# Performance work log

Measured on AMD Instinct MI355X. Metric: run time of the kernel, lower is better.

The kernel has to match this reference:

```python
import jax, jax.numpy as jnp
import numpy as np

B, T, C = 2, 2048, 1024
H = 16
D = C // H
E = 16
K = 2
THETA = 10000.0
ALPHA = 0.01
EPS = 1e-5


def rmsnorm(x, w):
    ms = jnp.mean(jnp.square(x), axis=-1, keepdims=True)
    return x * jax.lax.rsqrt(ms + EPS) * w


def rope_cos_sin(t_len, dim):
    # matches precompute_freqs_cis: freqs = theta**(-2i/dim), angles = t * freqs
    freqs = 1.0 / THETA ** (jnp.arange(0, dim // 2, dtype=jnp.float32) * 2.0 / dim)
    ang = jnp.arange(t_len, dtype=jnp.float32)[:, None] * freqs[None, :]  # [T, D/2]
    return jnp.cos(ang), jnp.sin(ang)


def apply_rope(x, cos, sin):
    # x: [B,T,H,D]; complex rotation on consecutive pairs (view_as_complex semantics)
    xr = x.reshape(x.shape[:-1] + (D // 2, 2))
    x0, x1 = xr[..., 0], xr[..., 1]
    c = cos[None, :, None, :]
    s = sin[None, :, None, :]
    return jnp.stack([x0 * c - x1 * s, x0 * s + x1 * c], axis=-1).reshape(x.shape)


def mlp(x, wf, bf, wp, bp):
    return jax.nn.silu(x @ wf + bf) @ wp + bp


def setup_inputs() -> dict:
    key = jax.random.key(0)
    ks = jax.random.split(key, 16)
    s = 0.02
    return {
        'x': jax.random.normal(ks[0], (B, T, C), jnp.float32),
        'ln1_w': jax.random.normal(ks[1], (C,), jnp.float32),
        'ln2_w': jax.random.normal(ks[2], (C,), jnp.float32),
        'w_attn': jax.random.normal(ks[3], (C, 3 * C), jnp.float32) * s,
        'b_attn': jnp.zeros((3 * C,), jnp.float32),
        'w_proj': jax.random.normal(ks[4], (C, C), jnp.float32) * s,
        'b_proj': jnp.zeros((C,), jnp.float32),
        'gate_w': jax.random.normal(ks[5], (E, C), jnp.float32) * s,
        'gate_bias': jnp.zeros((E,), jnp.float32),
        'exp_wf': jax.random.normal(ks[6], (E, C, 2 * C), jnp.float32) * s,
        'exp_bf': jnp.zeros((E, 2 * C), jnp.float32),
        'exp_wp': jax.random.normal(ks[7], (E, 2 * C, C), jnp.float32) * s,
        'exp_bp': jnp.zeros((E, C), jnp.float32),
        'sh_wf': jax.random.normal(ks[8], (C, 2 * C), jnp.float32) * s,
        'sh_bf': jnp.zeros((2 * C,), jnp.float32),
        'sh_wp': jax.random.normal(ks[9], (2 * C, C), jnp.float32) * s,
        'sh_bp': jnp.zeros((C,), jnp.float32),
    }


def reference(x, ln1_w, ln2_w, w_attn, b_attn, w_proj, b_proj, gate_w, gate_bias,
              exp_wf, exp_bf, exp_wp, exp_bp, sh_wf, sh_bf, sh_wp, sh_bp):
    # ---- attention sub-block ----
    h = rmsnorm(x, ln1_w)
    qkv = h @ w_attn + b_attn  # [B,T,3C]
    q, k, v = jnp.split(qkv, 3, axis=-1)
    q = q.reshape(B, T, H, D)
    k = k.reshape(B, T, H, D)
    v = v.reshape(B, T, H, D)
    cos, sin = rope_cos_sin(T, D)
    q = apply_rope(q, cos, sin)
    k = apply_rope(k, cos, sin)
    scores = jnp.einsum('bqhd,bkhd->bhqk', q, k) / jnp.sqrt(jnp.float32(D))
    causal = jnp.tril(jnp.ones((T, T), dtype=bool))
    scores = jnp.where(causal, scores, -jnp.inf)
    attn = jax.nn.softmax(scores, axis=-1)
    y = jnp.einsum('bhqk,bkhd->bqhd', attn, v).reshape(B, T, C)
    x = x + y @ w_proj + b_proj
    # ---- MoE sub-block ----
    h = rmsnorm(x, ln2_w).reshape(-1, C)  # [N,C]
    N = h.shape[0]
    logits = h @ gate_w.T
    p = jax.nn.softmax(logits.astype(jnp.float32), axis=-1)  # original_scores [N,E]
    _, idx = jax.lax.top_k(p + gate_bias, K)  # topk on biased scores
    w_sel = jnp.take_along_axis(p, idx, axis=-1)  # weights from unbiased scores [N,K]
    onehot = jax.nn.one_hot(idx, E, dtype=p.dtype)  # [N,K,E]
    w_dense = jnp.sum(onehot * w_sel[..., None], axis=1)  # [N,E] combine weights
    counts = jnp.sum(onehot, axis=(0, 1))  # bincount
    f_i = counts * E / (K * N + 1e-6)
    expert_probs = p.mean(axis=0)
    lb_loss = ALPHA * jnp.sum(f_i * expert_probs)
    out = jnp.zeros_like(h)
    for i in range(E):  # fixed small expert count
        out = out + mlp(h, exp_wf[i], exp_bf[i], exp_wp[i], exp_bp[i]) * w_dense[:, i:i + 1]
    out = out + mlp(h, sh_wf, sh_bf, sh_wp, sh_bp)
    return x + out.reshape(B, T, C), lb_loss
```

## Files before the change

kernel.cpp:

```cpp
#include <hip/hip_runtime.h>

typedef __bf16 bf16x8 __attribute__((ext_vector_type(8)));
typedef short  short8 __attribute__((ext_vector_type(8)));
typedef float  f32x4  __attribute__((ext_vector_type(4)));
typedef unsigned short u16;

#define NTOK 4096
#define TSEQ 2048
#define CDIM 1024
#define NEXP 16

__device__ __forceinline__ u16 f2bf(float f){
  union { float f; unsigned u; } v; v.f = f;
  unsigned r = v.u + 0x7fffu + ((v.u >> 16) & 1u);
  return (u16)(r >> 16);
}
__device__ __forceinline__ float bf2f(u16 u){
  union { unsigned u; float f; } v; v.u = ((unsigned)u) << 16; return v.f;
}

__device__ __forceinline__ f32x4 mfma16(short8 a, short8 b, f32x4 c){
  return __builtin_amdgcn_mfma_f32_16x16x32_bf16(
      __builtin_bit_cast(bf16x8, a), __builtin_bit_cast(bf16x8, b), c, 0, 0, 0);
}

__device__ __forceinline__ void gload_lds16(const void* g, void* l){
  __builtin_amdgcn_global_load_lds((__attribute__((address_space(1))) void*)g,
                                   (__attribute__((address_space(3))) void*)l,
                                   16, 0, 0);
}

__device__ __forceinline__ void tp_body(const float* __restrict__ in, u16* __restrict__ out,
                                        int K, int N, int k0, int n0, u16* lds16, int tid)
{
  int tx = tid & 15;
#pragma unroll
  for (int p = 0; p < 2; ++p) {
    int q = (tid >> 4) + p * 16;
    int k = 2 * q;
    float4 v0 = *(const float4*)(in + (size_t)(k0 + k)     * N + n0 + tx * 4);
    float4 v1 = *(const float4*)(in + (size_t)(k0 + k + 1) * N + n0 + tx * 4);
    const float* a0 = (const float*)&v0;
    const float* a1 = (const float*)&v1;
#pragma unroll
    for (int i = 0; i < 4; ++i) {
      unsigned val = (unsigned)f2bf(a0[i]) | ((unsigned)f2bf(a1[i]) << 16);
      *(unsigned*)&lds16[(tx * 4 + i) * 66 + k] = val;
    }
  }
  __syncthreads();
#pragma unroll
  for (int p = 0; p < 2; ++p) {
    int n = (tid >> 3) + p * 32;
    int k8 = (tid & 7) * 8;
    const unsigned* l32 = (const unsigned*)&lds16[n * 66 + k8];
    uint4 o4;
    o4.x = l32[0]; o4.y = l32[1]; o4.z = l32[2]; o4.w = l32[3];
    *(uint4*)(out + (size_t)(n0 + n) * K + k0 + k8) = o4;
  }
}

__global__ void transpose_wattn_k(const float* __restrict__ in, u16* __restrict__ out)
{
  __shared__ u16 lds16[64 * 66];
  int r = blockIdx.x;
  int n0 = (r % 48) * 64, k0 = (r / 48) * 64;
  tp_body(in, out, 1024, 3072, k0, n0, lds16, threadIdx.x);
}

__global__ void concat_bias_k(const float* __restrict__ exp_bf, const float* __restrict__ sh_bf,
                              const float* __restrict__ exp_bp, const float* __restrict__ sh_bp,
                              float* __restrict__ bf17, float* __restrict__ bp17)
{
  int i = blockIdx.x * 256 + threadIdx.x;
  if (i < 16 * 2048) bf17[i] = exp_bf[i];
  else if (i < 17 * 2048) bf17[i] = sh_bf[i - 16 * 2048];
  if (i < 16 * 1024) bp17[i] = exp_bp[i];
  else if (i < 17 * 1024) bp17[i] = sh_bp[i - 16 * 1024];
}

__global__ void rmsnorm_k(const float* __restrict__ x, const float* __restrict__ w,
                          u16* __restrict__ ob, float* __restrict__ of)
{
  int row = blockIdx.x, tid = threadIdx.x;
  const float4* xr = (const float4*)(x + (size_t)row * CDIM);
  float4 v = xr[tid];
  float ss = v.x*v.x + v.y*v.y + v.z*v.z + v.w*v.w;
  for (int d = 1; d < 64; d <<= 1) ss += __shfl_xor(ss, d);
  __shared__ float wacc[4];
  if ((tid & 63) == 0) wacc[tid >> 6] = ss;
  __syncthreads();
  float tot = wacc[0] + wacc[1] + wacc[2] + wacc[3];
  float scale = rsqrtf(tot * (1.0f / CDIM) + 1e-5f);
  float4 wv = ((const float4*)w)[tid];
  float o0 = v.x * scale * wv.x, o1 = v.y * scale * wv.y;
  float o2 = v.z * scale * wv.z, o3 = v.w * scale * wv.w;
  if (of) ((float4*)(of + (size_t)row * CDIM))[tid] = make_float4(o0, o1, o2, o3);
  ushort4 ov; ov.x = f2bf(o0); ov.y = f2bf(o1); ov.z = f2bf(o2); ov.w = f2bf(o3);
  ((ushort4*)(ob + (size_t)row * CDIM))[tid] = ov;
}

template<int MODE, int SWZ>
__global__ void __launch_bounds__(256, 4)
gemm_bt(const u16* __restrict__ A, int lda,
        const u16* __restrict__ Bt, long long bStrideZ,
        const float* __restrict__ bias, int biasStrideZ,
        void* __restrict__ Cout,
        const float* __restrict__ resid,
        int M, int N, int K,
        const int* __restrict__ counts, const int* __restrict__ offsets,
        const int* __restrict__ tokA, u16* __restrict__ vtp)
{
  int cb, rb, z;
  if (SWZ) {
    int nwg = gridDim.x * gridDim.y * gridDim.z;
    int d = (blockIdx.z * gridDim.y + blockIdx.y) * gridDim.x + blockIdx.x;
    int o = (d & 7) * (nwg >> 3) + (d >> 3);
    cb = o % gridDim.x;
    int t2 = o / gridDim.x;
    rb = t2 % gridDim.y;
    z  = t2 / gridDim.y;
  } else {
    cb = blockIdx.x; rb = blockIdx.y; z = blockIdx.z;
  }

  int mLoc = M, rowBase = 0;
  if (counts) { mLoc = counts[z]; rowBase = offsets[z]; }
  if (rb * 128 >= mLoc) return;

  const u16* Bz = Bt + (size_t)z * bStrideZ;
  const float* bz = bias + (size_t)z * biasStrideZ;

  __shared__ u16 lds_a[2][128 * 32];
  __shared__ u16 lds_b[2][128 * 32];

  int tid = threadIdx.x;
  int lane = tid & 63, wave = tid >> 6;
  int wm = wave >> 1, wn = wave & 1;
  int srow = wave * 16 + (lane >> 2);
  int skel = (lane & 3) * 8;
  int r16 = lane & 15, g8 = (lane >> 4) * 8;

  size_t arow[2];
  int ncol[2];
#pragma unroll
  for (int c = 0; c < 2; ++c) {
    int rloc = rb * 128 + c * 64 + srow;
    if (rloc >= mLoc) rloc = mLoc - 1;
    int grow = rowBase + rloc;
    arow[c] = tokA ? (size_t)tokA[grow] : (size_t)grow;
    ncol[c] = cb * 128 + c * 64 + srow;
  }

  f32x4 acc[4][4] = {};

  auto stage = [&](int kt, int buf){
    int k0 = kt * 32;
#pragma unroll
    for (int c = 0; c < 2; ++c) {
      gload_lds16(A + arow[c] * lda + k0 + skel,
                  (char*)&lds_a[buf][0] + c * 4096 + wave * 1024);
      gload_lds16(Bz + (size_t)ncol[c] * K + k0 + skel,
                  (char*)&lds_b[buf][0] + c * 4096 + wave * 1024);
    }
  };

  int nkt = K >> 5;
  stage(0, 0);
  for (int kt = 0; kt < nkt; ++kt) {
    int buf = kt & 1;
    if (kt + 1 < nkt) {
      stage(kt + 1, buf ^ 1);
      asm volatile("s_waitcnt vmcnt(4)" ::: "memory");
    } else {
      asm volatile("s_waitcnt vmcnt(0)" ::: "memory");
    }
    __builtin_amdgcn_s_barrier();
    short8 af[4], bfr[4];
#pragma unroll
    for (int i = 0; i < 4; ++i) {
      af[i]  = *(const short8*)&lds_a[buf][(wm * 64 + i * 16 + r16) * 32 + g8];
      bfr[i] = *(const short8*)&lds_b[buf][(wn * 64 + i * 16 + r16) * 32 + g8];
    }
#pragma unroll
    for (int i = 0; i < 4; ++i)
#pragma unroll
      for (int j = 0; j < 4; ++j)
        acc[i][j] = mfma16(af[i], bfr[j], acc[i][j]);
    __builtin_amdgcn_s_barrier();
  }

#pragma unroll
  for (int i = 0; i < 4; ++i) {
    int rl0 = rb * 128 + wm * 64 + i * 16 + (lane >> 4) * 4;
#pragma unroll
    for (int j = 0; j < 4; ++j) {
      int col = cb * 128 + wn * 64 + j * 16 + r16;
      float bv = bz[col];
#pragma unroll
      for (int r = 0; r < 4; ++r) {
        int rl = rl0 + r;
        if (rl >= mLoc) continue;
        int grow = rowBase + rl;
        float v = acc[i][j][r] + bv;
        if (MODE == 0) {
          ((float*)Cout)[(size_t)grow * N + col] = v;
        } else if (MODE == 1) {
          ((float*)Cout)[(size_t)grow * N + col] = v + resid[(size_t)grow * N + col];
        } else if (MODE == 2) {
          float s = v * (1.0f / (1.0f + __expf(-v)));
          ((u16*)Cout)[(size_t)grow * N + col] = f2bf(s);
        } else if (MODE == 4) {
          ((u16*)Cout)[(size_t)grow * N + col] = f2bf(v);
        } else {
          if (col < 2048) {
            ((float*)Cout)[(size_t)grow * N + col] = v;
          } else {
            int c10 = col - 2048;
            int h = c10 >> 6, dd = c10 & 63;
            int b = grow >> 11, t = grow & 2047;
            vtp[((size_t)(b * 16 + h) * 64 + dd) * TSEQ + t] = f2bf(v);
          }
        }
      }
    }
  }
}

__global__ void rope_qk_k(const float* __restrict__ qkv,
                          u16* __restrict__ qr, u16* __restrict__ kr)
{
  int flat = blockIdx.x * 256 + threadIdx.x;
  int i = flat & 31;
  int h = (flat >> 5) & 15;
  int n = flat >> 9;
  int b = n >> 11, t = n & 2047;
  const float* row = qkv + (size_t)n * 3072;
  float2 q = *(const float2*)(row + h * 64 + 2 * i);
  float2 k = *(const float2*)(row + 1024 + h * 64 + 2 * i);
  float freq = expf(-(float)i * (2.0f / 64.0f) * 9.210340371976184f);
  float ang = (float)t * freq;
  float sn, cs;
  sincosf(ang, &sn, &cs);
  float q0 = q.x * cs - q.y * sn, q1 = q.x * sn + q.y * cs;
  float k0 = k.x * cs - k.y * sn, k1 = k.x * sn + k.y * cs;
  int bh = b * 16 + h;
  size_t qoff = ((size_t)bh * TSEQ + t) * 64 + 2 * i;
  *(unsigned*)(qr + qoff) = (unsigned)f2bf(q0) | ((unsigned)f2bf(q1) << 16);
  *(unsigned*)(kr + qoff) = (unsigned)f2bf(k0) | ((unsigned)f2bf(k1) << 16);
}

__global__ void __launch_bounds__(512, 4)
attn_tp_k(const u16* __restrict__ qr, const u16* __restrict__ kr,
          const u16* __restrict__ vt, u16* __restrict__ y,
          const float* __restrict__ wProj, const float* __restrict__ shWf,
          const float* __restrict__ shWp,  const float* __restrict__ expWf,
          const float* __restrict__ expWp,
          u16* __restrict__ oProj, u16* __restrict__ oWf17, u16* __restrict__ oWp17)
{
  __shared__ union {
    struct { u16 lK[2][64 * 64]; u16 lV[2][64 * 64]; u16 plds[8][16 * 72]; } a;
    u16 t[2][64 * 66];
  } sm;

  int u = blockIdx.x;
  if (u >= 512) {
    int tid = threadIdx.x;
    int half = tid >> 8, t256 = tid & 255;
    int t = (u - 512) * 2 + half;
    const float* in; u16* out; int K, N, k0, n0;
    if (t < 8192) {
      int z = t >> 9, r = t & 511;
      in = expWf + (size_t)z * 2048 * 1024; out = oWf17 + (size_t)z * 2048 * 1024;
      K = 1024; N = 2048; n0 = (r & 31) * 64; k0 = (r >> 5) * 64;
    } else if (t < 16384) {
      int z = (t - 8192) >> 9, r = (t - 8192) & 511;
      in = expWp + (size_t)z * 2048 * 1024; out = oWp17 + (size_t)z * 2048 * 1024;
      K = 2048; N = 1024; n0 = (r & 15) * 64; k0 = (r >> 4) * 64;
    } else if (t < 16896) {
      int r = t - 16384;
      in = shWf; out = oWf17 + (size_t)16 * 2048 * 1024;
      K = 1024; N = 2048; n0 = (r & 31) * 64; k0 = (r >> 5) * 64;
    } else if (t < 17408) {
      int r = t - 16896;
      in = shWp; out = oWp17 + (size_t)16 * 2048 * 1024;
      K = 2048; N = 1024; n0 = (r & 15) * 64; k0 = (r >> 4) * 64;
    } else {
      int r = t - 17408;
      in = wProj; out = oProj; K = 1024; N = 1024; n0 = (r & 15) * 64; k0 = (r >> 4) * 64;
    }
    tp_body(in, out, K, N, k0, n0, &sm.t[half][0], t256);
    return;
  }

  int bh = u >> 4;
  int b = bh >> 4, h = bh & 15;
  int qb = 15 - (u & 15);
  int tid = threadIdx.x;
  int wv = tid >> 6, lane = tid & 63;
  int qrow0 = qb * 128 + wv * 16;
  const u16* qbase = qr + (size_t)bh * TSEQ * 64;
  const u16* kbase = kr + (size_t)bh * TSEQ * 64;
  const u16* vbase = vt + (size_t)bh * 64 * TSEQ;

  u16* pw = &sm.a.plds[wv][0];

  int r16 = lane & 15, g = lane >> 4;

  short8 aq0 = *(const short8*)(qbase + (size_t)(qrow0 + r16) * 64 + g * 8);
  short8 aq1 = *(const short8*)(qbase + (size_t)(qrow0 + r16) * 64 + 32 + g * 8);

  int sRow = tid >> 3;
  int sColE = (((tid & 7) * 16) ^ ((sRow & 7) << 4)) >> 1;

  float m[4] = {-1e30f, -1e30f, -1e30f, -1e30f};
  float l[4] = {0.f, 0.f, 0.f, 0.f};
  f32x4 o[4] = {};

  int nt = 2 * qb + 2;

  auto stage = [&](int t, int buf){
    int kp = t * 64;
    gload_lds16(kbase + ((size_t)(kp + sRow) << 6) + sColE,
                (char*)&sm.a.lK[buf][0] + wv * 1024);
    gload_lds16(vbase + (size_t)sRow * TSEQ + kp + sColE,
                (char*)&sm.a.lV[buf][0] + wv * 1024);
  };

  auto compute = [&](int t, int buf){
    int kp = t * 64;
    f32x4 s[4];
    __builtin_amdgcn_s_setprio(1);
#pragma unroll
    for (int st = 0; st < 4; ++st) {
      int rowK = st * 16 + r16;
      int sw = (rowK & 7) << 4;
      short8 kb0 = *(const short8*)((const char*)&sm.a.lK[buf][0] + rowK * 128 + ((g * 16) ^ sw));
      short8 kb1 = *(const short8*)((const char*)&sm.a.lK[buf][0] + rowK * 128 + ((64 + g * 16) ^ sw));
      f32x4 acc = {0.f, 0.f, 0.f, 0.f};
      acc = mfma16(aq0, kb0, acc);
      acc = mfma16(aq1, kb1, acc);
      s[st] = acc;
    }
    __builtin_amdgcn_s_setprio(0);

    float sc[4];
#pragma unroll
    for (int r = 0; r < 4; ++r) {
      int qpos = qrow0 + g * 4 + r;
      float v0 = (kp + r16      <= qpos) ? s[0][r] * 0.125f : -1e30f;
      float v1 = (kp + 16 + r16 <= qpos) ? s[1][r] * 0.125f : -1e30f;
      float v2 = (kp + 32 + r16 <= qpos) ? s[2][r] * 0.125f : -1e30f;
      float v3 = (kp + 48 + r16 <= qpos) ? s[3][r] * 0.125f : -1e30f;
      float mx = fmaxf(fmaxf(v0, v1), fmaxf(v2, v3));
      for (int d = 1; d < 16; d <<= 1) mx = fmaxf(mx, __shfl_xor(mx, d));
      float mnew = fmaxf(m[r], mx);
      float e0 = __expf(v0 - mnew), e1 = __expf(v1 - mnew);
      float e2 = __expf(v2 - mnew), e3 = __expf(v3 - mnew);
      float scale = __expf(m[r] - mnew);
      float rs = (e0 + e1) + (e2 + e3);
      for (int d = 1; d < 16; d <<= 1) rs += __shfl_xor(rs, d);
      l[r] = l[r] * scale + rs;
      m[r] = mnew;
      sc[r] = scale;
      int prow = (g * 4 + r) * 72;
      pw[prow + r16]      = f2bf(e0);
      pw[prow + 16 + r16] = f2bf(e1);
      pw[prow + 32 + r16] = f2bf(e2);
      pw[prow + 48 + r16] = f2bf(e3);
    }
#pragma unroll
    for (int c = 0; c < 4; ++c) {
      f32x4 t4 = o[c];
      t4[0] *= sc[0]; t4[1] *= sc[1]; t4[2] *= sc[2]; t4[3] *= sc[3];
      o[c] = t4;
    }

    short8 pa0 = *(const short8*)&pw[r16 * 72 + g * 8];
    short8 pa1 = *(const short8*)&pw[r16 * 72 + 32 + g * 8];
    __builtin_amdgcn_s_setprio(1);
#pragma unroll
    for (int c = 0; c < 4; ++c) {
      int rowV = c * 16 + r16;
      int sw = (rowV & 7) << 4;
      short8 vb0 = *(const short8*)((const char*)&sm.a.lV[buf][0] + rowV * 128 + ((g * 16) ^ sw));
      short8 vb1 = *(const short8*)((const char*)&sm.a.lV[buf][0] + rowV * 128 + ((64 + g * 16) ^ sw));
      o[c] = mfma16(pa0, vb0, o[c]);
      o[c] = mfma16(pa1, vb1, o[c]);
    }
    __builtin_amdgcn_s_setprio(0);
  };

  stage(0, 0);
  for (int t = 0; t < nt; ++t) {
    int buf = t & 1;
    if (t + 1 < nt) {
      stage(t + 1, buf ^ 1);
      asm volatile("s_waitcnt vmcnt(2)" ::: "memory");
    } else {
      asm volatile("s_waitcnt vmcnt(0)" ::: "memory");
    }
    __builtin_amdgcn_s_barrier();
    compute(t, buf);
    __builtin_amdgcn_s_barrier();
  }

#pragma unroll
  for (int c = 0; c < 4; ++c)
#pragma unroll
    for (int r = 0; r < 4; ++r) {
      int qpos = qrow0 + g * 4 + r;
      float val = o[c][r] / l[r];
      y[((size_t)(b * TSEQ + qpos)) * CDIM + h * 64 + c * 16 + r16] = f2bf(val);
    }
}

__global__ void zero_k(int* counts){
  int t = threadIdx.x;
  if (t < NEXP) counts[t] = 0;
  if (t == NEXP) counts[NEXP] = NTOK;
}

__global__ void gate_k(const float* __restrict__ h2, const float* __restrict__ gw,
                       const float* __restrict__ gb,
                       int* __restrict__ route_e, float* __restrict__ route_w,
                       int* __restrict__ counts, float* __restrict__ probs)
{
  int n = blockIdx.x, tid = threadIdx.x;
  __shared__ float hrow[CDIM];
  __shared__ float part[16][17];
  __shared__ float sm[16];
  ((float4*)hrow)[tid] = ((const float4*)(h2 + (size_t)n * CDIM))[tid];
  __syncthreads();
  int e = tid & 15, seg = tid >> 4;
  const float4* gw4 = (const float4*)(gw + (size_t)e * CDIM + seg * 64);
  const float4* hs4 = (const float4*)(hrow + seg * 64);
  float p = 0.f;
#pragma unroll
  for (int i = 0; i < 16; ++i) {
    float4 gv = gw4[i];
    float4 hv = hs4[i];
    p += hv.x * gv.x;
    p += hv.y * gv.y;
    p += hv.z * gv.z;
    p += hv.w * gv.w;
  }
  part[e][seg] = p;
  __syncthreads();
  if (tid < 16) {
    float lg = 0.f;
    for (int s = 0; s < 16; ++s) lg += part[tid][s];
    sm[tid] = lg;
  }
  __syncthreads();
  if (tid == 0) {
    float mx = sm[0];
    for (int i = 1; i < 16; ++i) mx = fmaxf(mx, sm[i]);
    float ssum = 0.f;
    for (int i = 0; i < 16; ++i) { float pe = expf(sm[i] - mx); sm[i] = pe; ssum += pe; }
    float inv = 1.0f / ssum;
    for (int i = 0; i < 16; ++i) sm[i] *= inv;
    int i1 = -1; float b1 = -1e30f;
    for (int i = 0; i < 16; ++i) { float t = sm[i] + gb[i]; if (t > b1) { b1 = t; i1 = i; } }
    int i2 = -1; float b2 = -1e30f;
    for (int i = 0; i < 16; ++i) { if (i == i1) continue; float t = sm[i] + gb[i]; if (t > b2) { b2 = t; i2 = i; } }
    route_e[2 * n] = i1; route_e[2 * n + 1] = i2;
    route_w[2 * n] = sm[i1]; route_w[2 * n + 1] = sm[i2];
    atomicAdd(&counts[i1], 1); atomicAdd(&counts[i2], 1);
  }
  __syncthreads();
  if (tid < 16) probs[(size_t)n * 16 + tid] = sm[tid];
}

__global__ void scan_k(const int* counts, int* offs, int* cursors){
  if (threadIdx.x == 0) {
    int acc = 0;
    for (int e = 0; e < NEXP; ++e) { offs[e] = acc; cursors[e] = acc; acc += counts[e]; }
    offs[NEXP] = acc;
  }
}

__global__ void fill_k(const int* __restrict__ route_e, const float* __restrict__ route_w,
                       int* __restrict__ cursors, int* __restrict__ tok, float* __restrict__ tw,
                       int* __restrict__ inv)
{
  int n = blockIdx.x * 256 + threadIdx.x;
  if (n >= NTOK) return;
  for (int j = 0; j < 2; ++j) {
    int e = route_e[2 * n + j];
    int pos = atomicAdd(&cursors[e], 1);
    tok[pos] = n; tw[pos] = route_w[2 * n + j];
    inv[2 * n + j] = pos;
  }
  tok[2 * NTOK + n] = n;
}

__global__ void combine_k(float* __restrict__ out, const float* __restrict__ x2,
                          const u16* __restrict__ eout,
                          const int* __restrict__ inv, const float* __restrict__ tw)
{
  int n = blockIdx.x, tid = threadIdx.x;
  int p0 = inv[2 * n], p1 = inv[2 * n + 1];
  float w0 = tw[p0], w1 = tw[p1];
  float4 xr = ((const float4*)(x2 + (size_t)n * CDIM))[tid];
  ushort4 es = ((const ushort4*)(eout + (size_t)(2 * NTOK + n) * CDIM))[tid];
  float4 a;
  a.x = xr.x + bf2f(es.x);
  a.y = xr.y + bf2f(es.y);
  a.z = xr.z + bf2f(es.z);
  a.w = xr.w + bf2f(es.w);
  ushort4 e0 = ((const ushort4*)(eout + (size_t)p0 * CDIM))[tid];
  ushort4 e1 = ((const ushort4*)(eout + (size_t)p1 * CDIM))[tid];
  a.x += bf2f(e0.x) * w0 + bf2f(e1.x) * w1;
  a.y += bf2f(e0.y) * w0 + bf2f(e1.y) * w1;
  a.z += bf2f(e0.z) * w0 + bf2f(e1.z) * w1;
  a.w += bf2f(e0.w) * w0 + bf2f(e1.w) * w1;
  ((float4*)(out + (size_t)n * CDIM))[tid] = a;
}

__global__ void lb2_k(const int* __restrict__ counts, const float* __restrict__ probs,
                      float* __restrict__ out)
{
  __shared__ float part[256][16];
  int t = threadIdx.x;
  float acc[16];
#pragma unroll
  for (int e = 0; e < 16; ++e) acc[e] = 0.f;
  for (int n = t; n < NTOK; n += 256) {
    const float4* row = (const float4*)(probs + (size_t)n * 16);
    float4 a0 = row[0], a1 = row[1], a2 = row[2], a3 = row[3];
    acc[0] += a0.x; acc[1] += a0.y; acc[2]  += a0.z; acc[3]  += a0.w;
    acc[4] += a1.x; acc[5] += a1.y; acc[6]  += a1.z; acc[7]  += a1.w;
    acc[8] += a2.x; acc[9] += a2.y; acc[10] += a2.z; acc[11] += a2.w;
    acc[12] += a3.x; acc[13] += a3.y; acc[14] += a3.z; acc[15] += a3.w;
  }
#pragma unroll
  for (int e = 0; e < 16; ++e) part[t][e] = acc[e];
  __syncthreads();
  __shared__ float colsum[16];
  if (t < 16) {
    float s = 0.f;
    for (int i = 0; i < 256; ++i) s += part[i][t];
    colsum[t] = s;
  }
  __syncthreads();
  if (t == 0) {
    float accl = 0.f;
    for (int e = 0; e < NEXP; ++e) {
      float f = (float)counts[e] * (16.0f / (2.0f * (float)NTOK + 1e-6f));
      accl += f * (colsum[e] * (1.0f / (float)NTOK));
    }
    out[0] = 0.01f * accl;
  }
}

extern "C" void kernel_launch(void* const* d_in, const int* in_sizes, int n_in,
                              void* d_out, int out_size, void* d_ws, size_t ws_size,
                              hipStream_t stream)
{
  const float* x      = (const float*)d_in[0];
  const float* ln1_w  = (const float*)d_in[1];
  const float* ln2_w  = (const float*)d_in[2];
  const float* w_attn = (const float*)d_in[3];
  const float* b_attn = (const float*)d_in[4];
  const float* w_proj = (const float*)d_in[5];
  const float* b_proj = (const float*)d_in[6];
  const float* gate_w = (const float*)d_in[7];
  const float* gate_b = (const float*)d_in[8];
  const float* exp_wf = (const float*)d_in[9];
  const float* exp_bf = (const float*)d_in[10];
  const float* exp_wp = (const float*)d_in[11];
  const float* exp_bp = (const float*)d_in[12];
  const float* sh_wf  = (const float*)d_in[13];
  const float* sh_bf  = (const float*)d_in[14];
  const float* sh_wp  = (const float*)d_in[15];
  const float* sh_bp  = (const float*)d_in[16];

  char* ws = (char*)d_ws;
  size_t off = 0;
  auto alloc = [&](size_t b){ size_t r = off; off = (off + b + 255) & ~(size_t)255; return r; };

  size_t oWAttnT = alloc(3072ull * 1024 * 2);
  size_t oWProjT = alloc(1024ull * 1024 * 2);
  size_t oExpWfT = alloc(17ull * 2048 * 1024 * 2);
  size_t oExpWpT = alloc(17ull * 1024 * 2048 * 2);
  size_t oX2     = alloc(4096ull * 1024 * 4);
  size_t oH2F    = alloc(4096ull * 1024 * 4);
  size_t oH2B    = alloc(4096ull * 1024 * 2);
  size_t oQKV    = alloc(4096ull * 3072 * 4);
  size_t oQR     = alloc(4096ull * 1024 * 2);
  size_t oKR     = alloc(4096ull * 1024 * 2);
  size_t oVT     = alloc(4096ull * 1024 * 2);
  size_t oH1B    = alloc(4096ull * 1024 * 2);
  size_t oCnt    = alloc(128);
  size_t oOffs   = alloc(128);
  size_t oCurs   = alloc(128);
  size_t oRE     = alloc(8192ull * 4);
  size_t oRW     = alloc(8192ull * 4);
  size_t oTok    = alloc(12288ull * 4);
  size_t oTw     = alloc(8192ull * 4);
  size_t oInv    = alloc(8192ull * 4);
  size_t oProbs  = alloc(4096ull * 16 * 4);
  size_t oBf17   = alloc(17ull * 2048 * 4);
  size_t oBp17   = alloc(17ull * 1024 * 4);

  u16* pWAttnT = (u16*)(ws + oWAttnT);
  u16* pWProjT = (u16*)(ws + oWProjT);
  u16* pWf17   = (u16*)(ws + oExpWfT);
  u16* pWp17   = (u16*)(ws + oExpWpT);
  float* pX2   = (float*)(ws + oX2);
  float* pH2F  = (float*)(ws + oH2F);
  u16* pH2B    = (u16*)(ws + oH2B);
  float* pQKV  = (float*)(ws + oQKV);
  u16* pHid17  = (u16*)(ws + oQKV);
  u16* pQR     = (u16*)(ws + oQR);
  u16* pKR     = (u16*)(ws + oKR);
  u16* pVT     = (u16*)(ws + oVT);
  u16* pH1B    = (u16*)(ws + oH1B);
  u16* pY      = (u16*)(ws + oH1B);
  u16* pEoutB  = (u16*)(ws + oQR);
  int* pCnt    = (int*)(ws + oCnt);
  int* pOffs   = (int*)(ws + oOffs);
  int* pCurs   = (int*)(ws + oCurs);
  int* pRE     = (int*)(ws + oRE);
  float* pRW   = (float*)(ws + oRW);
  int* pTok    = (int*)(ws + oTok);
  float* pTw   = (float*)(ws + oTw);
  int* pInv    = (int*)(ws + oInv);
  float* pProbs= (float*)(ws + oProbs);
  float* pBf17 = (float*)(ws + oBf17);
  float* pBp17 = (float*)(ws + oBp17);

  transpose_wattn_k<<<768, 256, 0, stream>>>(w_attn, pWAttnT);
  concat_bias_k<<<(17 * 2048 + 255) / 256, 256, 0, stream>>>(exp_bf, sh_bf, exp_bp, sh_bp, pBf17, pBp17);

  rmsnorm_k<<<NTOK, 256, 0, stream>>>(x, ln1_w, pH1B, nullptr);

  gemm_bt<5, 1><<<dim3(3072/128, NTOK/128, 1), 256, 0, stream>>>(
      pH1B, 1024, pWAttnT, 0, b_attn, 0, pQKV, nullptr,
      NTOK, 3072, 1024, nullptr, nullptr, nullptr, pVT);

  rope_qk_k<<<(NTOK * 16 * 32) / 256, 256, 0, stream>>>(pQKV, pQR, pKR);

  attn_tp_k<<<512 + 8832, 512, 0, stream>>>(pQR, pKR, pVT, pY,
                                            w_proj, sh_wf, sh_wp, exp_wf, exp_wp,
                                            pWProjT, pWf17, pWp17);

  gemm_bt<1, 1><<<dim3(1024/128, NTOK/128, 1), 256, 0, stream>>>(
      pY, 1024, pWProjT, 0, b_proj, 0, pX2, x,
      NTOK, 1024, 1024, nullptr, nullptr, nullptr, nullptr);

  rmsnorm_k<<<NTOK, 256, 0, stream>>>(pX2, ln2_w, pH2B, pH2F);

  zero_k<<<1, 64, 0, stream>>>(pCnt);
  gate_k<<<NTOK, 256, 0, stream>>>(pH2F, gate_w, gate_b, pRE, pRW, pCnt, pProbs);
  scan_k<<<1, 64, 0, stream>>>(pCnt, pOffs, pCurs);
  fill_k<<<NTOK/256, 256, 0, stream>>>(pRE, pRW, pCurs, pTok, pTw, pInv);
  lb2_k<<<1, 256, 0, stream>>>(pCnt, pProbs, ((float*)d_out) + (size_t)NTOK * CDIM);

  gemm_bt<2, 0><<<dim3(2048/128, NTOK/128, 17), 256, 0, stream>>>(
      pH2B, 1024, pWf17, 2048ll * 1024, pBf17, 2048, pHid17, nullptr,
      NTOK, 2048, 1024, pCnt, pOffs, pTok, nullptr);

  gemm_bt<4, 0><<<dim3(1024/128, NTOK/128, 17), 256, 0, stream>>>(
      pHid17, 2048, pWp17, 2048ll * 1024, pBp17, 1024, pEoutB, nullptr,
      NTOK, 1024, 2048, pCnt, pOffs, nullptr, nullptr);

  combine_k<<<NTOK, 256, 0, stream>>>((float*)d_out, pX2, pEoutB, pInv, pTw);

  (void)in_sizes; (void)n_in; (void)out_size; (void)ws_size;
}
```

Measured before the change: 636.7 us.

## Fuse second RMSNorm with MoE gate and reorder attention block mapping

Merges the post-attention RMSNorm and the router/gate kernel into one kernel, so the fp32 normalized activations stay in shared memory instead of being written to and read back from global memory. Zeroing the expert counters moves into the bias-concatenation kernel, which removes a separate launch. The attention block index mapping is also changed so consecutive blocks walk across batch-heads for the same query block rather than across query blocks within one head. This is meant to balance causal work across CUs and improve K/V cache sharing.

```diff
diff --git a/kernel.cpp b/kernel.cpp
--- a/kernel.cpp
+++ b/kernel.cpp
@@ -70,17 +70,20 @@
 
 __global__ void concat_bias_k(const float* __restrict__ exp_bf, const float* __restrict__ sh_bf,
                               const float* __restrict__ exp_bp, const float* __restrict__ sh_bp,
-                              float* __restrict__ bf17, float* __restrict__ bp17)
+                              float* __restrict__ bf17, float* __restrict__ bp17,
+                              int* __restrict__ counts)
 {
   int i = blockIdx.x * 256 + threadIdx.x;
   if (i < 16 * 2048) bf17[i] = exp_bf[i];
   else if (i < 17 * 2048) bf17[i] = sh_bf[i - 16 * 2048];
   if (i < 16 * 1024) bp17[i] = exp_bp[i];
   else if (i < 17 * 1024) bp17[i] = sh_bp[i - 16 * 1024];
+  if (blockIdx.x == 0 && threadIdx.x <= NEXP)
+    counts[threadIdx.x] = (threadIdx.x == NEXP) ? NTOK : 0;
 }
 
 __global__ void rmsnorm_k(const float* __restrict__ x, const float* __restrict__ w,
-                          u16* __restrict__ ob, float* __restrict__ of)
+                          u16* __restrict__ ob)
 {
   int row = blockIdx.x, tid = threadIdx.x;
   const float4* xr = (const float4*)(x + (size_t)row * CDIM);
@@ -95,9 +98,76 @@
   float4 wv = ((const float4*)w)[tid];
   float o0 = v.x * scale * wv.x, o1 = v.y * scale * wv.y;
   float o2 = v.z * scale * wv.z, o3 = v.w * scale * wv.w;
-  if (of) ((float4*)(of + (size_t)row * CDIM))[tid] = make_float4(o0, o1, o2, o3);
   ushort4 ov; ov.x = f2bf(o0); ov.y = f2bf(o1); ov.z = f2bf(o2); ov.w = f2bf(o3);
   ((ushort4*)(ob + (size_t)row * CDIM))[tid] = ov;
+}
+
+__global__ void rmsnorm_gate_k(const float* __restrict__ x2, const float* __restrict__ w,
+                               const float* __restrict__ gw, const float* __restrict__ gb,
+                               u16* __restrict__ ob,
+                               int* __restrict__ route_e, float* __restrict__ route_w,
+                               int* __restrict__ counts, float* __restrict__ probs)
+{
+  int row = blockIdx.x, tid = threadIdx.x;
+  __shared__ float hrow[CDIM];
+  __shared__ float wacc[4];
+  __shared__ float part[16][17];
+  __shared__ float sm[16];
+
+  const float4* xr = (const float4*)(x2 + (size_t)row * CDIM);
+  float4 v = xr[tid];
+  float ss = v.x*v.x + v.y*v.y + v.z*v.z + v.w*v.w;
+  for (int d = 1; d < 64; d <<= 1) ss += __shfl_xor(ss, d);
+  if ((tid & 63) == 0) wacc[tid >> 6] = ss;
+  __syncthreads();
+  float tot = wacc[0] + wacc[1] + wacc[2] + wacc[3];
+  float scale = rsqrtf(tot * (1.0f / CDIM) + 1e-5f);
+  float4 wv = ((const float4*)w)[tid];
+  float o0 = v.x * scale * wv.x, o1 = v.y * scale * wv.y;
+  float o2 = v.z * scale * wv.z, o3 = v.w * scale * wv.w;
+  ((float4*)hrow)[tid] = make_float4(o0, o1, o2, o3);
+  ushort4 ov; ov.x = f2bf(o0); ov.y = f2bf(o1); ov.z = f2bf(o2); ov.w = f2bf(o3);
+  ((ushort4*)(ob + (size_t)row * CDIM))[tid] = ov;
+  __syncthreads();
+
+  int e = tid & 15, seg = tid >> 4;
+  const float4* gw4 = (const float4*)(gw + (size_t)e * CDIM + seg * 64);
+  const float4* hs4 = (const float4*)(hrow + seg * 64);
+  float p = 0.f;
+#pragma unroll
+  for (int i = 0; i < 16; ++i) {
+    float4 gv = gw4[i];
+    float4 hv = hs4[i];
+    p += hv.x * gv.x;
+    p += hv.y * gv.y;
+    p += hv.z * gv.z;
+    p += hv.w * gv.w;
+  }
+  part[e][seg] = p;
+  __syncthreads();
+  if (tid < 16) {
+    float lg = 0.f;
+    for (int s = 0; s < 16; ++s) lg += part[tid][s];
+    sm[tid] = lg;
+  }
+  __syncthreads();
+  if (tid == 0) {
+    float mx = sm[0];
+    for (int i = 1; i < 16; ++i) mx = fmaxf(mx, sm[i]);
+    float ssum = 0.f;
+    for (int i = 0; i < 16; ++i) { float pe = expf(sm[i] - mx); sm[i] = pe; ssum += pe; }
+    float inv = 1.0f / ssum;
+    for (int i = 0; i < 16; ++i) sm[i] *= inv;
+    int i1 = -1; float b1 = -1e30f;
+    for (int i = 0; i < 16; ++i) { float t = sm[i] + gb[i]; if (t > b1) { b1 = t; i1 = i; } }
+    int i2 = -1; float b2 = -1e30f;
+    for (int i = 0; i < 16; ++i) { if (i == i1) continue; float t = sm[i] + gb[i]; if (t > b2) { b2 = t; i2 = i; } }
+    route_e[2 * row] = i1; route_e[2 * row + 1] = i2;
+    route_w[2 * row] = sm[i1]; route_w[2 * row + 1] = sm[i2];
+    atomicAdd(&counts[i1], 1); atomicAdd(&counts[i2], 1);
+  }
+  __syncthreads();
+  if (tid < 16) probs[(size_t)row * 16 + tid] = sm[tid];
 }
 
 template<int MODE, int SWZ>
@@ -293,9 +363,10 @@
     return;
   }
 
-  int bh = u >> 4;
+  int j  = u >> 5;
+  int bh = u & 31;
   int b = bh >> 4, h = bh & 15;
-  int qb = 15 - (u & 15);
+  int qb = 15 - j;
   int tid = threadIdx.x;
   int wv = tid >> 6, lane = tid & 63;
   int qrow0 = qb * 128 + wv * 16;
@@ -415,63 +486,6 @@
     }
 }
 
-__global__ void zero_k(int* counts){
-  int t = threadIdx.x;
-  if (t < NEXP) counts[t] = 0;
-  if (t == NEXP) counts[NEXP] = NTOK;
-}
-
-__global__ void gate_k(const float* __restrict__ h2, const float* __restrict__ gw,
-                       const float* __restrict__ gb,
-                       int* __restrict__ route_e, float* __restrict__ route_w,
-                       int* __restrict__ counts, float* __restrict__ probs)
-{
-  int n = blockIdx.x, tid = threadIdx.x;
-  __shared__ float hrow[CDIM];
-  __shared__ float part[16][17];
-  __shared__ float sm[16];
-  ((float4*)hrow)[tid] = ((const float4*)(h2 + (size_t)n * CDIM))[tid];
-  __syncthreads();
-  int e = tid & 15, seg = tid >> 4;
-  const float4* gw4 = (const float4*)(gw + (size_t)e * CDIM + seg * 64);
-  const float4* hs4 = (const float4*)(hrow + seg * 64);
-  float p = 0.f;
-#pragma unroll
-  for (int i = 0; i < 16; ++i) {
-    float4 gv = gw4[i];
-    float4 hv = hs4[i];
-    p += hv.x * gv.x;
-    p += hv.y * gv.y;
-    p += hv.z * gv.z;
-    p += hv.w * gv.w;
-  }
-  part[e][seg] = p;
-  __syncthreads();
-  if (tid < 16) {
-    float lg = 0.f;
-    for (int s = 0; s < 16; ++s) lg += part[tid][s];
-    sm[tid] = lg;
-  }
-  __syncthreads();
-  if (tid == 0) {
-    float mx = sm[0];
-    for (int i = 1; i < 16; ++i) mx = fmaxf(mx, sm[i]);
-    float ssum = 0.f;
-    for (int i = 0; i < 16; ++i) { float pe = expf(sm[i] - mx); sm[i] = pe; ssum += pe; }
-    float inv = 1.0f / ssum;
-    for (int i = 0; i < 16; ++i) sm[i] *= inv;
-    int i1 = -1; float b1 = -1e30f;
-    for (int i = 0; i < 16; ++i) { float t = sm[i] + gb[i]; if (t > b1) { b1 = t; i1 = i; } }
-    int i2 = -1; float b2 = -1e30f;
-    for (int i = 0; i < 16; ++i) { if (i == i1) continue; float t = sm[i] + gb[i]; if (t > b2) { b2 = t; i2 = i; } }
-    route_e[2 * n] = i1; route_e[2 * n + 1] = i2;
-    route_w[2 * n] = sm[i1]; route_w[2 * n + 1] = sm[i2];
-    atomicAdd(&counts[i1], 1); atomicAdd(&counts[i2], 1);
-  }
-  __syncthreads();
-  if (tid < 16) probs[(size_t)n * 16 + tid] = sm[tid];
-}
-
 __global__ void scan_k(const int* counts, int* offs, int* cursors){
   if (threadIdx.x == 0) {
     int acc = 0;
@@ -585,7 +599,6 @@
   size_t oExpWfT = alloc(17ull * 2048 * 1024 * 2);
   size_t oExpWpT = alloc(17ull * 1024 * 2048 * 2);
   size_t oX2     = alloc(4096ull * 1024 * 4);
-  size_t oH2F    = alloc(4096ull * 1024 * 4);
   size_t oH2B    = alloc(4096ull * 1024 * 2);
   size_t oQKV    = alloc(4096ull * 3072 * 4);
   size_t oQR     = alloc(4096ull * 1024 * 2);
@@ -609,7 +622,6 @@
   u16* pWf17   = (u16*)(ws + oExpWfT);
   u16* pWp17   = (u16*)(ws + oExpWpT);
   float* pX2   = (float*)(ws + oX2);
-  float* pH2F  = (float*)(ws + oH2F);
   u16* pH2B    = (u16*)(ws + oH2B);
   float* pQKV  = (float*)(ws + oQKV);
   u16* pHid17  = (u16*)(ws + oQKV);
@@ -632,9 +644,10 @@
   float* pBp17 = (float*)(ws + oBp17);
 
   transpose_wattn_k<<<768, 256, 0, stream>>>(w_attn, pWAttnT);
-  concat_bias_k<<<(17 * 2048 + 255) / 256, 256, 0, stream>>>(exp_bf, sh_bf, exp_bp, sh_bp, pBf17, pBp17);
-
-  rmsnorm_k<<<NTOK, 256, 0, stream>>>(x, ln1_w, pH1B, nullptr);
+  concat_bias_k<<<(17 * 2048 + 255) / 256, 256, 0, stream>>>(exp_bf, sh_bf, exp_bp, sh_bp,
+                                                             pBf17, pBp17, pCnt);
+
+  rmsnorm_k<<<NTOK, 256, 0, stream>>>(x, ln1_w, pH1B);
 
   gemm_bt<5, 1><<<dim3(3072/128, NTOK/128, 1), 256, 0, stream>>>(
       pH1B, 1024, pWAttnT, 0, b_attn, 0, pQKV, nullptr,
@@ -650,10 +663,9 @@
       pY, 1024, pWProjT, 0, b_proj, 0, pX2, x,
       NTOK, 1024, 1024, nullptr, nullptr, nullptr, nullptr);
 
-  rmsnorm_k<<<NTOK, 256, 0, stream>>>(pX2, ln2_w, pH2B, pH2F);
-
-  zero_k<<<1, 64, 0, stream>>>(pCnt);
-  gate_k<<<NTOK, 256, 0, stream>>>(pH2F, gate_w, gate_b, pRE, pRW, pCnt, pProbs);
+  rmsnorm_gate_k<<<NTOK, 256, 0, stream>>>(pX2, ln2_w, gate_w, gate_b,
+                                           pH2B, pRE, pRW, pCnt, pProbs);
+
   scan_k<<<1, 64, 0, stream>>>(pCnt, pOffs, pCurs);
   fill_k<<<NTOK/256, 256, 0, stream>>>(pRE, pRW, pCurs, pTok, pTw, pInv);
   lb2_k<<<1, 256, 0, stream>>>(pCnt, pProbs, ((float*)d_out) + (size_t)NTOK * CDIM);
```

Measured after the change: 591.0 us. -7.2%, faster.
